# Performance work log

Hardware: AMD Instinct MI355X
Metric: run time of the kernel (lower is better)

Reference implementation:

```python
import jax, jax.numpy as jnp
import numpy as np

THRESH = 0.59275  # PercolationQ default threshold
SIZES = list(range(3, 42, 2))  # 20 Chebyshev scales
B, P, C = 16, 100, 3


def _connected_components(imgs):
    # imgs: (N, s, s) int32 in {0,1}. 4-connectivity CC via min-label propagation.
    # Label value = (min flat index in component) + 1, background = 0.
    N, s, _ = imgs.shape
    big = s * s + 1
    fg = imgs > 0
    idx = jnp.arange(s * s, dtype=jnp.int32).reshape(1, s, s) + 1
    init = jnp.where(fg, idx, big)

    def body(state):
        L, _ = state
        Lp = jnp.pad(L, ((0, 0), (1, 1), (1, 1)), constant_values=big)
        m = jnp.minimum(jnp.minimum(Lp[:, :-2, 1:-1], Lp[:, 2:, 1:-1]),
                        jnp.minimum(Lp[:, 1:-1, :-2], Lp[:, 1:-1, 2:]))
        Ln = jnp.where(fg, jnp.minimum(L, m), big)
        return Ln, jnp.any(Ln != L)

    L, _ = jax.lax.while_loop(lambda st: st[1], body, (init, jnp.bool_(True)))
    return jnp.where(fg, L, 0)


def _scale_features(x):
    b, p, s, _, c = x.shape
    # --- Chebyshev layer (faithful to the TF reshape + center-crop semantics) ---
    r = x.reshape(b * s, p, s, c)
    center = r[:, (p - 1) // 2, (s - 1) // 2, :][:, None, None, :]
    binm = (jnp.abs(r - center).max(axis=3) <= float(s)).astype(jnp.int32).reshape(b, p, s, s)
    # --- Probability: histogram of per-patch foreground counts ---
    counts = binm.sum(axis=(2, 3))  # (b, p), values in [0, s^2]
    L = s * s + 1
    hist = jax.vmap(lambda cc: jnp.bincount(cc, length=L))(counts).astype(jnp.float32) / p
    numbers = jnp.concatenate([jnp.ones((1,), jnp.float32), jnp.arange(1, L, dtype=jnp.float32)])
    # --- FractalDimension / Lacunarity ---
    fd = (hist / numbers).sum(axis=1)
    mu1 = (hist * numbers).sum(axis=1) ** 2
    mu2 = (hist * numbers ** 2).sum(axis=1)
    lac = (mu2 - mu1) / mu1
    # --- PercolationQ ---
    pq = ((counts.astype(jnp.float32) / (s * s)) >= THRESH).astype(jnp.float32).mean(axis=1)
    # --- Clusterize (tfa semantics: labels unique/consecutive across the whole batch) ---
    labels = _connected_components(binm.reshape(b * p, s, s))
    lhist = jax.vmap(lambda l: jnp.bincount(l.ravel(), length=L))(labels)  # (b*p, s^2+1)
    ncomp = (lhist[:, 1:] > 0).sum(axis=1)
    # max global label in image i = cumulative component count (0 if no components)
    maxlab = jnp.where(ncomp > 0, jnp.cumsum(ncomp), 0)
    pc = maxlab.astype(jnp.float32).reshape(b, p).mean(axis=1)
    # PercolationM: max bincount over per-sample flattened global labels
    #   = max(total background pixels, largest component size in the sample)
    bg = lhist[:, 0].reshape(b, p).sum(axis=1)
    maxcomp = lhist[:, 1:].max(axis=1).reshape(b, p).max(axis=1)
    pm = jnp.maximum(bg, maxcomp).astype(jnp.float32)
    return fd, lac, pq, pc, pm


def _forward(xs):
    feats = [_scale_features(x) for x in xs]
    fd = jnp.stack([f[0] for f in feats], axis=1)
    lac = jnp.stack([f[1] for f in feats], axis=1)
    pq = jnp.stack([f[2] for f in feats], axis=1)
    pc = jnp.stack([f[3] for f in feats], axis=1)
    pm = jnp.stack([f[4] for f in feats], axis=1)
    out = jnp.concatenate([pc, pq, pm, lac, fd], axis=1)  # (B, 100)
    return out.reshape(-1, 10, 10)


def setup_inputs() -> dict:
    key = jax.random.key(0)
    inp = {}
    for i, s in enumerate(SIZES):
        inp[f"x{i}"] = jax.random.normal(jax.random.fold_in(key, i), (B, P, s, s, C), dtype=jnp.float32)
    return inp


def reference(x0, x1, x2, x3, x4, x5, x6, x7, x8, x9, x10, x11, x12, x13, x14, x15, x16, x17, x18, x19):
    return _forward([x0, x1, x2, x3, x4, x5, x6, x7, x8, x9, x10, x11, x12, x13, x14, x15, x16, x17, x18, x19])
```

## Files before the change

### kernel.cpp

```cpp
#include <hip/hip_runtime.h>

#define NSCALES 20
#define BATCH 16
#define PATCH 100
#define IMGS_PER_SCALE 1600
#define TOTAL_IMGS 32000
#define THREADS 256
#define CHUNKPX 4096
#define MAXIMG 512
#define S2MAX 1681

struct Ptrs   { const float* p[NSCALES]; };
struct Starts { int blkStart[NSCALES]; };

__global__ __launch_bounds__(THREADS)
void count_kernel(Ptrs ptrs, Starts st, int* __restrict__ wsCounts)
{
    const int bid = blockIdx.x;
    int sc = 0;
    #pragma unroll
    for (int k = 1; k < NSCALES; k++) sc += (bid >= st.blkStart[k]) ? 1 : 0;
    const int s  = 3 + 2 * sc;
    const int s2 = s * s;
    const float* __restrict__ x = ptrs.p[sc];
    const unsigned mS   = 0xFFFFFFFFu / (unsigned)s + 1;
    const unsigned m100 = 0xFFFFFFFFu / 100u + 1;
    const int Ntot = IMGS_PER_SCALE * s2;
    const int P0   = (bid - st.blkStart[sc]) * CHUNKPX;
    const int Pend = min(P0 + CHUNKPX, Ntot);
    const int tid  = threadIdx.x;

    __shared__ float cenL[18 * 3];
    __shared__ int   cntL[MAXIMG];

    const int M0      = (int)__umulhi((unsigned)P0, mS);
    const int Mlast   = (int)__umulhi((unsigned)(Pend - 1), mS);
    const int imgBase = (int)__umulhi((unsigned)M0, mS);
    const int imgLast = (int)__umulhi((unsigned)Mlast, mS);
    const int j0      = (int)__umulhi((unsigned)M0, m100);
    const int jEnd    = (int)__umulhi((unsigned)Mlast, m100);
    const int nImg = imgLast - imgBase + 1;
    const int nj   = jEnd - j0 + 1;

    for (int t = tid; t < nj * 3; t += THREADS) {
        int j  = j0 + t / 3;
        int ch = t - (t / 3) * 3;
        cenL[t] = x[(size_t)(((j * PATCH + 49) * s + (s >> 1)) * 3 + ch)];
    }
    for (int t = tid; t < nImg; t += THREADS) cntL[t] = 0;
    __syncthreads();

    const float fs = (float)s;
    #pragma unroll
    for (int it = 0; it < CHUNKPX / 4 / THREADS; it++) {
        const int pc = P0 + (tid + it * THREADS) * 4;
        const bool act = (pc < Pend);
        int iA = -1, cA = 0, iB = -1, cB = 0;
        if (act) {
            const float4* q4 = (const float4*)(x + (size_t)pc * 3);
            float4 a = q4[0], b = q4[1], c = q4[2];
            float v0=a.x,v1=a.y,v2=a.z,v3=a.w,v4=b.x,v5=b.y,v6=b.z,v7=b.w,
                  v8=c.x,v9=c.y,v10=c.z,v11=c.w;
            int im[4], fg[4];
            #pragma unroll
            for (int q = 0; q < 4; q++) {
                int P   = pc + q;
                int M   = (int)__umulhi((unsigned)P, mS);
                int img = (int)__umulhi((unsigned)M, mS);
                int j   = (int)__umulhi((unsigned)M, m100);
                const float* ce = &cenL[(j - j0) * 3];
                float p0 = (q==0)?v0:(q==1)?v3:(q==2)?v6:v9;
                float p1 = (q==0)?v1:(q==1)?v4:(q==2)?v7:v10;
                float p2 = (q==0)?v2:(q==1)?v5:(q==2)?v8:v11;
                float d = fmaxf(fmaxf(fabsf(p0 - ce[0]), fabsf(p1 - ce[1])),
                                fabsf(p2 - ce[2]));
                im[q] = img;
                fg[q] = (d <= fs) ? 1 : 0;
            }
            iA = im[0]; cA = fg[0];
            #pragma unroll
            for (int q = 1; q < 4; q++) {
                if (im[q] == iA) cA += fg[q];
                else { iB = im[q]; cB += fg[q]; }
            }
        }
        unsigned long long am = __ballot(act);
        if (am == ~0ull) {
            int first = __shfl(iA, 0);
            int lastA = __shfl(iA, 63), lastB = __shfl(iB, 63);
            int last  = (lastB >= 0) ? lastB : lastA;
            if (last - first <= 1) {
                int tot  = cA + cB;
                int low  = ((iA == first) ? cA : 0) + ((iB == first) ? cB : 0);
                int high = tot - low;
                #pragma unroll
                for (int mm = 32; mm >= 1; mm >>= 1) {
                    low  += __shfl_xor(low, mm);
                    high += __shfl_xor(high, mm);
                }
                if ((tid & 63) == 0) {
                    atomicAdd(&cntL[first - imgBase], low);
                    if (high > 0) atomicAdd(&cntL[first + 1 - imgBase], high);
                }
                continue;
            }
        }
        if (iA >= 0) atomicAdd(&cntL[iA - imgBase], cA);
        if (iB >= 0) atomicAdd(&cntL[iB - imgBase], cB);
    }
    __syncthreads();

    for (int t = tid; t < nImg; t += THREADS) {
        int img = imgBase + t;
        int lo = img * s2, hi = lo + s2;
        int g = sc * IMGS_PER_SCALE + img;
        int v = cntL[t];
        if (lo >= P0 && hi <= Pend) wsCounts[g] = v;
        else atomicAdd(&wsCounts[g], v);
    }
}

__global__ __launch_bounds__(THREADS)
void cc_kernel(Ptrs ptrs, const int* __restrict__ wsCounts,
               int* __restrict__ wsNcomp, int* __restrict__ wsMaxc)
{
    const int bid = blockIdx.x;
    const int sc  = bid / 25;
    const int s   = 3 + 2 * sc;
    const int s2  = s * s;
    const int BIGL = s2 + 1;
    const float* __restrict__ x = ptrs.p[sc];
    const int imgLoc0 = (bid % 25) * 64;
    const int tid = threadIdx.x;
    const unsigned mS = 0xFFFFFFFFu / (unsigned)s + 1;

    __shared__ int slowList[64];
    __shared__ int nslow;
    __shared__ int lab[S2MAX];
    __shared__ int szh[S2MAX];
    __shared__ int redN[4], redM[4];

    if (tid == 0) nslow = 0;
    __syncthreads();
    if (tid < 64) {
        int img = imgLoc0 + tid;
        int g = sc * IMGS_PER_SCALE + img;
        int c = wsCounts[g];
        if (c == s2)      { wsNcomp[g] = 1; wsMaxc[g] = s2; }
        else if (c == 0)  { wsNcomp[g] = 0; wsMaxc[g] = 0; }
        else { int k = atomicAdd(&nslow, 1); slowList[k] = img; }
    }
    __syncthreads();
    const int ns = nslow;
    if (ns == 0) return;

    if (s2 <= 64) {
        const int w = tid >> 6, l = tid & 63;
        for (int idx = w; idx < ns; idx += 4) {
            int img = slowList[idx];
            int fg = 0, labr = BIGL, i1 = 0, i2 = 0;
            if (l < s2) {
                i1 = (int)__umulhi((unsigned)l, mS);
                i2 = l - i1 * s;
                int M = img * s + i1;
                int j = M / PATCH;
                const float* ce = x + (size_t)(((j * PATCH + 49) * s + (s >> 1)) * 3);
                const float* px = x + ((size_t)img * s2 + l) * 3;
                float d = fmaxf(fmaxf(fabsf(px[0] - ce[0]), fabsf(px[1] - ce[1])),
                                fabsf(px[2] - ce[2]));
                if (d <= (float)s) { fg = 1; labr = l + 1; }
            }
            for (;;) {
                int m = labr;
                int vU = __shfl(labr, (l - s) & 63);
                int vD = __shfl(labr, (l + s) & 63);
                int vL = __shfl(labr, (l - 1) & 63);
                int vR = __shfl(labr, (l + 1) & 63);
                if (fg) {
                    if (i1 > 0)     m = min(m, vU);
                    if (i1 < s - 1) m = min(m, vD);
                    if (i2 > 0)     m = min(m, vL);
                    if (i2 < s - 1) m = min(m, vR);
                }
                int vJ = __shfl(labr, (m - 1) & 63);
                if (fg) m = min(m, vJ);
                unsigned long long chg = __ballot(m < labr);
                labr = m;
                if (chg == 0) break;
            }
            int ncomp = __popcll(__ballot(fg && labr == l + 1));
            int mc = 0;
            for (int r = 0; r < s2; r++) {
                int szr = __popcll(__ballot(fg && labr == r + 1));
                mc = max(mc, szr);
            }
            if (l == 0) {
                int g = sc * IMGS_PER_SCALE + img;
                wsNcomp[g] = ncomp; wsMaxc[g] = mc;
            }
        }
    } else {
        for (int idx = 0; idx < ns; idx++) {
            int img = slowList[idx];
            const int ibase = img * s2 * 3;
            for (int i = tid; i < s2; i += THREADS) {
                int i1 = (int)__umulhi((unsigned)i, mS);
                int M = img * s + i1;
                int j = M / PATCH;
                const float* ce = x + (size_t)(((j * PATCH + 49) * s + (s >> 1)) * 3);
                const float* px = x + ibase + i * 3;
                float d = fmaxf(fmaxf(fabsf(px[0] - ce[0]), fabsf(px[1] - ce[1])),
                                fabsf(px[2] - ce[2]));
                lab[i] = (d <= (float)s) ? (i + 1) : BIGL;
                szh[i] = 0;
            }
            __syncthreads();
            for (;;) {
                bool changed = false;
                for (int i = tid; i < s2; i += THREADS) {
                    int L0 = lab[i];
                    if (L0 <= s2) {
                        int i1 = (int)__umulhi((unsigned)i, mS);
                        int i2 = i - i1 * s;
                        int m = L0;
                        if (i1 > 0)     m = min(m, lab[i - s]);
                        if (i1 < s - 1) m = min(m, lab[i + s]);
                        if (i2 > 0)     m = min(m, lab[i - 1]);
                        if (i2 < s - 1) m = min(m, lab[i + 1]);
                        m = min(m, lab[m - 1]);
                        if (m < L0) { lab[i] = m; changed = true; }
                    }
                }
                if (__syncthreads_count(changed ? 1 : 0) == 0) break;
            }
            int ncomp = 0;
            for (int i = tid; i < s2; i += THREADS) {
                int L = lab[i];
                if (L <= s2) {
                    atomicAdd(&szh[L - 1], 1);
                    if (L == i + 1) ncomp++;
                }
            }
            __syncthreads();
            int mc = 0;
            for (int i = tid; i < s2; i += THREADS) mc = max(mc, szh[i]);
            for (int m = 32; m >= 1; m >>= 1) {
                ncomp += __shfl_xor(ncomp, m);
                mc     = max(mc, __shfl_xor(mc, m));
            }
            int wid = tid >> 6, lane = tid & 63;
            if (lane == 0) { redN[wid] = ncomp; redM[wid] = mc; }
            __syncthreads();
            if (tid == 0) {
                int g = sc * IMGS_PER_SCALE + img;
                wsNcomp[g] = redN[0] + redN[1] + redN[2] + redN[3];
                wsMaxc[g]  = max(max(redM[0], redM[1]), max(redM[2], redM[3]));
            }
            __syncthreads();
        }
    }
}

__global__ __launch_bounds__(THREADS)
void final_kernel(const int* __restrict__ wsCounts,
                  const int* __restrict__ wsNcomp,
                  const int* __restrict__ wsMaxc,
                  float* __restrict__ out)
{
    const int scale = blockIdx.x;
    const int s  = 3 + 2 * scale;
    const int s2 = s * s;
    const int tid = threadIdx.x;
    const int NB = IMGS_PER_SCALE;
    const int CH = 7;

    __shared__ int nc[IMGS_PER_SCALE];
    __shared__ int tsum[THREADS];

    for (int i = tid; i < NB; i += THREADS) nc[i] = wsNcomp[scale * NB + i];
    __syncthreads();

    int lsum = 0;
    for (int k = 0; k < CH; k++) {
        int idx = tid * CH + k;
        if (idx < NB) lsum += nc[idx];
    }
    tsum[tid] = lsum;
    __syncthreads();
    for (int st = 1; st < THREADS; st <<= 1) {
        int v = (tid >= st) ? tsum[tid - st] : 0;
        __syncthreads();
        tsum[tid] += v;
        __syncthreads();
    }
    int run = (tid > 0) ? tsum[tid - 1] : 0;
    for (int k = 0; k < CH; k++) {
        int idx = tid * CH + k;
        if (idx < NB) {
            int v = nc[idx];
            run += v;
            nc[idx] = (v > 0) ? run : 0;
        }
    }
    __syncthreads();

    int b    = tid >> 4;
    int lane = tid & 15;
    float fdsum = 0.f, sn = 0.f, sn2 = 0.f, pcsum = 0.f;
    int pqc = 0, bg = 0, mcx = 0;
    for (int q = lane; q < PATCH; q += 16) {
        int i = b * PATCH + q;
        int c = wsCounts[scale * NB + i];
        float n = (c > 0) ? (float)c : 1.0f;
        fdsum += 1.0f / n;
        sn    += n;
        sn2   += n * n;
        pqc   += ((float)c / (float)s2 >= 0.59275f) ? 1 : 0;
        bg    += (s2 - c);
        mcx    = max(mcx, wsMaxc[scale * NB + i]);
        pcsum += (float)nc[i];
    }
    for (int m = 8; m >= 1; m >>= 1) {
        fdsum += __shfl_xor(fdsum, m);
        sn    += __shfl_xor(sn, m);
        sn2   += __shfl_xor(sn2, m);
        pcsum += __shfl_xor(pcsum, m);
        pqc   += __shfl_xor(pqc, m);
        bg    += __shfl_xor(bg, m);
        mcx    = max(mcx, __shfl_xor(mcx, m));
    }
    if (lane == 0) {
        float fd  = fdsum / 100.0f;
        float m1  = sn / 100.0f;
        float mu1 = m1 * m1;
        float mu2 = sn2 / 100.0f;
        float lac = (mu2 - mu1) / mu1;
        float pq  = (float)pqc / 100.0f;
        float pc  = pcsum / 100.0f;
        float pm  = (float)max(bg, mcx);
        out[b * 100 +  0 + scale] = pc;
        out[b * 100 + 20 + scale] = pq;
        out[b * 100 + 40 + scale] = pm;
        out[b * 100 + 60 + scale] = lac;
        out[b * 100 + 80 + scale] = fd;
    }
}

extern "C" void kernel_launch(void* const* d_in, const int* in_sizes, int n_in,
                              void* d_out, int out_size, void* d_ws, size_t ws_size,
                              hipStream_t stream)
{
    Ptrs ptrs;
    for (int i = 0; i < NSCALES; i++) ptrs.p[i] = (const float*)d_in[i];

    Starts st;
    int acc = 0;
    for (int i = 0; i < NSCALES; i++) {
        st.blkStart[i] = acc;
        int s = 3 + 2 * i, s2 = s * s;
        acc += (IMGS_PER_SCALE * s2 + CHUNKPX - 1) / CHUNKPX;
    }

    int* wsC = (int*)d_ws;
    int* wsN = wsC + TOTAL_IMGS;
    int* wsM = wsN + TOTAL_IMGS;

    hipMemsetAsync(wsC, 0, TOTAL_IMGS * sizeof(int), stream);
    count_kernel<<<acc, THREADS, 0, stream>>>(ptrs, st, wsC);
    cc_kernel<<<TOTAL_IMGS / 64, THREADS, 0, stream>>>(ptrs, wsC, wsN, wsM);
    final_kernel<<<NSCALES, THREADS, 0, stream>>>(wsC, wsN, wsM, (float*)d_out);
}
```

Baseline: 74.05 us.

## Specialize count kernel per scale and replace memset+global atomics with split partial counts

The per-pixel count kernel is templated on the scale size so index divisions become compile-time constants. Each thread now processes 16 contiguous pixels with wide loads, and the wave-level ballot reduction is dropped. Boundary images write their partial counts into two separate slots that the next kernel sums, which removes the workspace memset and the global atomics. This costs extra workspace and more register pressure from 12 float4 loads per thread.

```diff
diff --git a/kernel.cpp b/kernel.cpp
--- a/kernel.cpp
+++ b/kernel.cpp
@@ -1,127 +1,127 @@
 #include <hip/hip_runtime.h>
 
 #define NSCALES 20
-#define BATCH 16
 #define PATCH 100
 #define IMGS_PER_SCALE 1600
 #define TOTAL_IMGS 32000
 #define THREADS 256
-#define CHUNKPX 4096
-#define MAXIMG 512
+#define PXT 16
+#define CHUNKPX (THREADS * PXT)
+#define MAXIMG 464
 #define S2MAX 1681
 
 struct Ptrs   { const float* p[NSCALES]; };
 struct Starts { int blkStart[NSCALES]; };
 
+template<int S>
+__device__ __forceinline__ void count_body(const float* __restrict__ x,
+                                           int blkLocal, int sc,
+                                           int* __restrict__ wsC2,
+                                           float4* cenL, int* cntL)
+{
+    constexpr int S2 = S * S;
+    constexpr int ROWDIV = 100 * S;
+    const int Ntot = IMGS_PER_SCALE * S2;
+    const int P0   = blkLocal * CHUNKPX;
+    const int Pend = min(P0 + CHUNKPX, Ntot);
+    const int tid  = threadIdx.x;
+
+    const int imgBase = P0 / S2;
+    const int imgLast = (Pend - 1) / S2;
+    const int nImg    = imgLast - imgBase + 1;
+    const int j0      = P0 / ROWDIV;
+    const int jEnd    = (Pend - 1) / ROWDIV;
+    const int nj      = jEnd - j0 + 1;
+
+    if (tid < nj) {
+        int j = j0 + tid;
+        const float* c = x + (size_t)(((j * PATCH + 49) * S + (S >> 1)) * 3);
+        cenL[tid] = make_float4(c[0], c[1], c[2], 0.f);
+    }
+    for (int t = tid; t < nImg; t += THREADS) cntL[t] = 0;
+    __syncthreads();
+
+    const int p0 = P0 + tid * PXT;
+    if (p0 < Pend) {
+        const float4* q4 = (const float4*)(x + (size_t)p0 * 3);
+        float4 v[12];
+        #pragma unroll
+        for (int q = 0; q < 12; q++) v[q] = q4[q];
+        const float* f = (const float*)v;
+
+        const int iA = p0 / S2;
+        const int r0 = p0 - iA * S2;
+        const int jA = p0 / ROWDIV;
+        const int jB = (p0 + PXT - 1) / ROWDIV;
+        const float4 ceA = cenL[jA - j0];
+        const float4 ceB = (jB != jA) ? cenL[jB - j0] : ceA;
+        const int flip = (jB != jA) ? ((jA + 1) * ROWDIV - p0) : PXT;
+
+        int cA = 0, cB = 0, cC = 0;
+        #pragma unroll
+        for (int q = 0; q < PXT; q++) {
+            const float4 ce = (q < flip) ? ceA : ceB;
+            float d = fmaxf(fmaxf(fabsf(f[q*3+0] - ce.x),
+                                  fabsf(f[q*3+1] - ce.y)),
+                            fabsf(f[q*3+2] - ce.z));
+            int fg = (d <= (float)S) ? 1 : 0;
+            int t  = r0 + q;
+            if constexpr (S2 >= PXT) {
+                cA += (t < S2) ? fg : 0;
+                cB += (t >= S2) ? fg : 0;
+            } else {
+                cA += (t < S2) ? fg : 0;
+                cB += (t >= S2 && t < 2 * S2) ? fg : 0;
+                cC += (t >= 2 * S2) ? fg : 0;
+            }
+        }
+        atomicAdd(&cntL[iA - imgBase], cA);
+        if (cB) atomicAdd(&cntL[iA + 1 - imgBase], cB);
+        if constexpr (S2 < PXT) {
+            if (cC) atomicAdd(&cntL[iA + 2 - imgBase], cC);
+        }
+    }
+    __syncthreads();
+
+    for (int t = tid; t < nImg; t += THREADS) {
+        int img = imgBase + t;
+        int lo = img * S2, hi = lo + S2;
+        int g = sc * IMGS_PER_SCALE + img;
+        int vv = cntL[t];
+        if (lo >= P0) {
+            wsC2[2 * g] = vv;
+            if (hi <= Pend) wsC2[2 * g + 1] = 0;
+        } else {
+            wsC2[2 * g + 1] = vv;
+        }
+    }
+}
+
 __global__ __launch_bounds__(THREADS)
-void count_kernel(Ptrs ptrs, Starts st, int* __restrict__ wsCounts)
+void count_kernel(Ptrs ptrs, Starts st, int* __restrict__ wsC2)
 {
     const int bid = blockIdx.x;
     int sc = 0;
     #pragma unroll
     for (int k = 1; k < NSCALES; k++) sc += (bid >= st.blkStart[k]) ? 1 : 0;
-    const int s  = 3 + 2 * sc;
-    const int s2 = s * s;
-    const float* __restrict__ x = ptrs.p[sc];
-    const unsigned mS   = 0xFFFFFFFFu / (unsigned)s + 1;
-    const unsigned m100 = 0xFFFFFFFFu / 100u + 1;
-    const int Ntot = IMGS_PER_SCALE * s2;
-    const int P0   = (bid - st.blkStart[sc]) * CHUNKPX;
-    const int Pend = min(P0 + CHUNKPX, Ntot);
-    const int tid  = threadIdx.x;
-
-    __shared__ float cenL[18 * 3];
-    __shared__ int   cntL[MAXIMG];
-
-    const int M0      = (int)__umulhi((unsigned)P0, mS);
-    const int Mlast   = (int)__umulhi((unsigned)(Pend - 1), mS);
-    const int imgBase = (int)__umulhi((unsigned)M0, mS);
-    const int imgLast = (int)__umulhi((unsigned)Mlast, mS);
-    const int j0      = (int)__umulhi((unsigned)M0, m100);
-    const int jEnd    = (int)__umulhi((unsigned)Mlast, m100);
-    const int nImg = imgLast - imgBase + 1;
-    const int nj   = jEnd - j0 + 1;
-
-    for (int t = tid; t < nj * 3; t += THREADS) {
-        int j  = j0 + t / 3;
-        int ch = t - (t / 3) * 3;
-        cenL[t] = x[(size_t)(((j * PATCH + 49) * s + (s >> 1)) * 3 + ch)];
-    }
-    for (int t = tid; t < nImg; t += THREADS) cntL[t] = 0;
-    __syncthreads();
-
-    const float fs = (float)s;
-    #pragma unroll
-    for (int it = 0; it < CHUNKPX / 4 / THREADS; it++) {
-        const int pc = P0 + (tid + it * THREADS) * 4;
-        const bool act = (pc < Pend);
-        int iA = -1, cA = 0, iB = -1, cB = 0;
-        if (act) {
-            const float4* q4 = (const float4*)(x + (size_t)pc * 3);
-            float4 a = q4[0], b = q4[1], c = q4[2];
-            float v0=a.x,v1=a.y,v2=a.z,v3=a.w,v4=b.x,v5=b.y,v6=b.z,v7=b.w,
-                  v8=c.x,v9=c.y,v10=c.z,v11=c.w;
-            int im[4], fg[4];
-            #pragma unroll
-            for (int q = 0; q < 4; q++) {
-                int P   = pc + q;
-                int M   = (int)__umulhi((unsigned)P, mS);
-                int img = (int)__umulhi((unsigned)M, mS);
-                int j   = (int)__umulhi((unsigned)M, m100);
-                const float* ce = &cenL[(j - j0) * 3];
-                float p0 = (q==0)?v0:(q==1)?v3:(q==2)?v6:v9;
-                float p1 = (q==0)?v1:(q==1)?v4:(q==2)?v7:v10;
-                float p2 = (q==0)?v2:(q==1)?v5:(q==2)?v8:v11;
-                float d = fmaxf(fmaxf(fabsf(p0 - ce[0]), fabsf(p1 - ce[1])),
-                                fabsf(p2 - ce[2]));
-                im[q] = img;
-                fg[q] = (d <= fs) ? 1 : 0;
-            }
-            iA = im[0]; cA = fg[0];
-            #pragma unroll
-            for (int q = 1; q < 4; q++) {
-                if (im[q] == iA) cA += fg[q];
-                else { iB = im[q]; cB += fg[q]; }
-            }
-        }
-        unsigned long long am = __ballot(act);
-        if (am == ~0ull) {
-            int first = __shfl(iA, 0);
-            int lastA = __shfl(iA, 63), lastB = __shfl(iB, 63);
-            int last  = (lastB >= 0) ? lastB : lastA;
-            if (last - first <= 1) {
-                int tot  = cA + cB;
-                int low  = ((iA == first) ? cA : 0) + ((iB == first) ? cB : 0);
-                int high = tot - low;
-                #pragma unroll
-                for (int mm = 32; mm >= 1; mm >>= 1) {
-                    low  += __shfl_xor(low, mm);
-                    high += __shfl_xor(high, mm);
-                }
-                if ((tid & 63) == 0) {
-                    atomicAdd(&cntL[first - imgBase], low);
-                    if (high > 0) atomicAdd(&cntL[first + 1 - imgBase], high);
-                }
-                continue;
-            }
-        }
-        if (iA >= 0) atomicAdd(&cntL[iA - imgBase], cA);
-        if (iB >= 0) atomicAdd(&cntL[iB - imgBase], cB);
-    }
-    __syncthreads();
-
-    for (int t = tid; t < nImg; t += THREADS) {
-        int img = imgBase + t;
-        int lo = img * s2, hi = lo + s2;
-        int g = sc * IMGS_PER_SCALE + img;
-        int v = cntL[t];
-        if (lo >= P0 && hi <= Pend) wsCounts[g] = v;
-        else atomicAdd(&wsCounts[g], v);
+    const int blkLocal = bid - st.blkStart[sc];
+
+    __shared__ float4 cenL[16];
+    __shared__ int    cntL[MAXIMG];
+
+    switch (sc) {
+#define CASE(i) case i: count_body<3 + 2*(i)>(ptrs.p[i], blkLocal, i, wsC2, cenL, cntL); break;
+        CASE(0)  CASE(1)  CASE(2)  CASE(3)  CASE(4)
+        CASE(5)  CASE(6)  CASE(7)  CASE(8)  CASE(9)
+        CASE(10) CASE(11) CASE(12) CASE(13) CASE(14)
+        CASE(15) CASE(16) CASE(17) CASE(18) CASE(19)
+#undef CASE
     }
 }
 
 __global__ __launch_bounds__(THREADS)
-void cc_kernel(Ptrs ptrs, const int* __restrict__ wsCounts,
+void cc_kernel(Ptrs ptrs, const int* __restrict__ wsC2,
+               int* __restrict__ wsCnt,
                int* __restrict__ wsNcomp, int* __restrict__ wsMaxc)
 {
     const int bid = blockIdx.x;
@@ -145,7 +145,8 @@
     if (tid < 64) {
         int img = imgLoc0 + tid;
         int g = sc * IMGS_PER_SCALE + img;
-        int c = wsCounts[g];
+        int c = wsC2[2 * g] + wsC2[2 * g + 1];
+        wsCnt[g] = c;
         if (c == s2)      { wsNcomp[g] = 1; wsMaxc[g] = s2; }
         else if (c == 0)  { wsNcomp[g] = 0; wsMaxc[g] = 0; }
         else { int k = atomicAdd(&nslow, 1); slowList[k] = img; }
@@ -262,7 +263,7 @@
 }
 
 __global__ __launch_bounds__(THREADS)
-void final_kernel(const int* __restrict__ wsCounts,
+void final_kernel(const int* __restrict__ wsCnt,
                   const int* __restrict__ wsNcomp,
                   const int* __restrict__ wsMaxc,
                   float* __restrict__ out)
@@ -310,7 +311,7 @@
     int pqc = 0, bg = 0, mcx = 0;
     for (int q = lane; q < PATCH; q += 16) {
         int i = b * PATCH + q;
-        int c = wsCounts[scale * NB + i];
+        int c = wsCnt[scale * NB + i];
         float n = (c > 0) ? (float)c : 1.0f;
         fdsum += 1.0f / n;
         sn    += n;
@@ -361,12 +362,12 @@
         acc += (IMGS_PER_SCALE * s2 + CHUNKPX - 1) / CHUNKPX;
     }
 
-    int* wsC = (int*)d_ws;
-    int* wsN = wsC + TOTAL_IMGS;
-    int* wsM = wsN + TOTAL_IMGS;
-
-    hipMemsetAsync(wsC, 0, TOTAL_IMGS * sizeof(int), stream);
-    count_kernel<<<acc, THREADS, 0, stream>>>(ptrs, st, wsC);
-    cc_kernel<<<TOTAL_IMGS / 64, THREADS, 0, stream>>>(ptrs, wsC, wsN, wsM);
-    final_kernel<<<NSCALES, THREADS, 0, stream>>>(wsC, wsN, wsM, (float*)d_out);
-}
+    int* wsC2  = (int*)d_ws;
+    int* wsCnt = wsC2 + 2 * TOTAL_IMGS;
+    int* wsN   = wsCnt + TOTAL_IMGS;
+    int* wsM   = wsN + TOTAL_IMGS;
+
+    count_kernel<<<acc, THREADS, 0, stream>>>(ptrs, st, wsC2);
+    cc_kernel<<<TOTAL_IMGS / 64, THREADS, 0, stream>>>(ptrs, wsC2, wsCnt, wsN, wsM);
+    final_kernel<<<NSCALES, THREADS, 0, stream>>>(wsCnt, wsN, wsM, (float*)d_out);
+}
```

Result: faster. 67.68 us (-8.6%).
